# Optimization experiments

Hardware: AMD Instinct MI355X
Metric: run time of the kernel (lower is better)

The kernel has to match this reference:

```python
import jax, jax.numpy as jnp
import numpy as np

B, S, D, M = 4, 2048, 1024, 4  # batch, seq_len, d_model, n_stride_masks


def setup_inputs() -> dict:
    key = jax.random.key(0)
    ks = jax.random.split(key, 10)
    lin = lambda k: jax.random.normal(k, (D, D), jnp.float32) / np.float32(np.sqrt(D))
    return {
        "x": jax.random.normal(ks[0], (B, S, D), jnp.float32),
        "stride_masks": jax.random.randint(ks[1], (M, S, S), 0, 2, jnp.int32),
        "Wq": lin(ks[2]), "bq": jnp.zeros((D,), jnp.float32),
        "Wk": lin(ks[3]), "bk": jnp.zeros((D,), jnp.float32),
        "Wv": lin(ks[4]), "bv": jnp.zeros((D,), jnp.float32),
        "Wo": lin(ks[5]), "bo": jnp.zeros((D,), jnp.float32),
    }


def reference(x, stride_masks, Wq, bq, Wk, bk, Wv, bv, Wo, bo):
    scale = jnp.float32(np.sqrt(D))
    Q = x @ Wq + bq  # [B,S,D]
    K = x @ Wk + bk
    V = x @ Wv + bv
    # scores are identical for every mask; compute once (same math as the loop)
    scores = jnp.einsum("bqd,bkd->bqk", Q, K) / scale  # [B,S,S]
    masked = jnp.where(stride_masks[:, None] == 0, jnp.float32(-1e9), scores[None])  # [M,B,S,S]
    weights = jax.nn.softmax(masked, axis=-1)
    # sum over masks then divide by M == mean(stack(outs), 0)
    out = jnp.einsum("mbqk,bkd->bqd", weights, V) / jnp.float32(M)
    return out @ Wo + bo
```

## Files before the change

kernel.cpp:

```cpp
#include <hip/hip_runtime.h>
#include <hip/hip_bf16.h>
#include <stdint.h>

#define B_ 4
#define S_ 2048
#define D_ 1024
#define M_ 4

typedef __bf16 bf16;
typedef _Float16 f16;
typedef unsigned char u8;
typedef __bf16 bf16x8 __attribute__((ext_vector_type(8)));
typedef _Float16 f16x8 __attribute__((ext_vector_type(8)));
typedef float f32x4 __attribute__((ext_vector_type(4)));

__device__ __forceinline__ void async_copy16(const void* g, void* l) {
  __builtin_amdgcn_global_load_lds(
      (const __attribute__((address_space(1))) void*)g,
      (__attribute__((address_space(3))) void*)l, 16, 0, 0);
}

__global__ __launch_bounds__(256) void prep(
    const float* __restrict__ x, const float* __restrict__ w0,
    const float* __restrict__ w1, const float* __restrict__ w2,
    const float* __restrict__ w3, const int* __restrict__ masks,
    bf16* __restrict__ xc, bf16* __restrict__ WT, u8* __restrict__ pk) {
  __shared__ bf16 t[64][65];
  const int blk = blockIdx.x;
  const int tid = threadIdx.x;
  const long SS = (long)S_ * S_;

  if (blk < 4096) {
    const long i = (long)blk * 2048 + tid * 8;
    const float4 a = *(const float4*)(x + i);
    const float4 b = *(const float4*)(x + i + 4);
    bf16x8 o;
    o[0] = (bf16)a.x; o[1] = (bf16)a.y; o[2] = (bf16)a.z; o[3] = (bf16)a.w;
    o[4] = (bf16)b.x; o[5] = (bf16)b.y; o[6] = (bf16)b.z; o[7] = (bf16)b.w;
    *(bf16x8*)(xc + i) = o;
  } else if (blk < 5120) {
    const int local = blk - 4096;
    const int z = local >> 8;
    const int rem = local & 255;
    const int r0 = (rem >> 4) * 64;
    const int c0 = (rem & 15) * 64;
    const int tx = tid & 63;
    const int ty = tid >> 6;
    const float* in = (z == 0) ? w0 : (z == 1) ? w1 : (z == 2) ? w2 : w3;
    bf16* out = WT + (long)z * D_ * D_;
    for (int i = ty; i < 64; i += 4)
      t[i][tx] = (bf16)in[(long)(r0 + i) * D_ + c0 + tx];
    __syncthreads();
    for (int i = ty; i < 64; i += 4)
      out[(long)(c0 + i) * D_ + r0 + tx] = t[tx][i];
  } else {
    const long e = (long)(blk - 5120) * 2048 + tid * 8;
    unsigned long long wv = 0;
#pragma unroll
    for (int m = 0; m < M_; ++m) {
      const int4 a = *(const int4*)(masks + m * SS + e);
      const int4 b = *(const int4*)(masks + m * SS + e + 4);
      const int v[8] = {a.x, a.y, a.z, a.w, b.x, b.y, b.z, b.w};
#pragma unroll
      for (int j = 0; j < 8; ++j)
        wv |= (unsigned long long)(v[j] != 0 ? 1u : 0u) << (8 * j + m);
    }
    *(unsigned long long*)(pk + e) = wv;
  }
}

__global__ __launch_bounds__(256) void transposeB(
    const bf16* __restrict__ in, bf16* __restrict__ out,
    int rows, int cols, long ib, long ob) {
  __shared__ bf16 t[64][65];
  in += (long)blockIdx.z * ib;
  out += (long)blockIdx.z * ob;
  const int r0 = blockIdx.y * 64;
  const int c0 = blockIdx.x * 64;
  const int tx = threadIdx.x & 63;
  const int ty = threadIdx.x >> 6;
#pragma unroll
  for (int i = ty; i < 64; i += 4) t[i][tx] = in[(long)(r0 + i) * cols + c0 + tx];
  __syncthreads();
#pragma unroll
  for (int i = ty; i < 64; i += 4) out[(long)(c0 + i) * rows + r0 + tx] = t[tx][i];
}

#define MODE_PLAIN 0
#define MODE_EXP 1
#define MODE_QKV 2

template <typename OutT, int MODE>
__global__ __launch_bounds__(256) void gemm_bt(
    const bf16* __restrict__ A, long aB, int lda,
    const bf16* __restrict__ Bt, long bB, int ldb,
    OutT* __restrict__ C, long cB, int ldc,
    const float* __restrict__ bias0, const float* __restrict__ bias1,
    const float* __restrict__ bias2, float alpha, int K) {
  __shared__ __align__(16) bf16 As[2][128 * 64];
  __shared__ __align__(16) bf16 Bs[2][128 * 64];
  const int tid = threadIdx.x;
  const int lane = tid & 63;
  const int w = tid >> 6;
  const int wm = w & 1;
  const int wn = w >> 1;
  A += (long)blockIdx.z * aB;
  Bt += (long)blockIdx.z * bB;
  if (MODE != MODE_QKV) C += (long)blockIdx.z * cB;

  const int gx = gridDim.x;
  const int pid = blockIdx.y * gx + blockIdx.x;
  const int gsz = 16 * gx;
  const int bym = (pid / gsz) * 16 + (pid % 16);
  const int bxm = (pid % gsz) / 16;

  const int row0 = bym * 128;
  const int col0 = bxm * 128;
  const int quad = lane >> 4;
  const int l15 = lane & 15;
  const int srow = lane >> 3;
  const int scol = (lane & 7) * 8;

  f32x4 acc[4][4];
#pragma unroll
  for (int i = 0; i < 4; ++i)
#pragma unroll
    for (int j = 0; j < 4; ++j) acc[i][j] = (f32x4){0.f, 0.f, 0.f, 0.f};

  const int nk = K >> 6;

#pragma unroll
  for (int c = 0; c < 4; ++c) {
    const int r = c * 32 + w * 8;
    async_copy16(A + (long)(row0 + r + srow) * lda + scol, &As[0][r * 64]);
    async_copy16(Bt + (long)(col0 + r + srow) * ldb + scol, &Bs[0][r * 64]);
  }

  for (int i = 0; i < nk; ++i) {
    const int cur = i & 1;
    __syncthreads();
    if (i + 1 < nk) {
      const int kt = (i + 1) << 6;
      const int nxt = cur ^ 1;
#pragma unroll
      for (int c = 0; c < 4; ++c) {
        const int r = c * 32 + w * 8;
        async_copy16(A + (long)(row0 + r + srow) * lda + kt + scol, &As[nxt][r * 64]);
        async_copy16(Bt + (long)(col0 + r + srow) * ldb + kt + scol, &Bs[nxt][r * 64]);
      }
    }
#pragma unroll
    for (int ks = 0; ks < 2; ++ks) {
      bf16x8 af[4], bf[4];
#pragma unroll
      for (int j = 0; j < 4; ++j) {
        af[j] = *(const bf16x8*)&As[cur][(wm * 64 + j * 16 + l15) * 64 + ks * 32 + quad * 8];
        bf[j] = *(const bf16x8*)&Bs[cur][(wn * 64 + j * 16 + l15) * 64 + ks * 32 + quad * 8];
      }
#pragma unroll
      for (int mi = 0; mi < 4; ++mi)
#pragma unroll
        for (int ni = 0; ni < 4; ++ni)
          acc[mi][ni] = __builtin_amdgcn_mfma_f32_16x16x32_bf16(af[mi], bf[ni], acc[mi][ni], 0, 0, 0);
    }
  }

  const int grp = (MODE == MODE_QKV) ? (bxm >> 3) : 0;
  const float* bias = (MODE == MODE_QKV)
                          ? (grp == 0 ? bias0 : grp == 1 ? bias1 : bias2)
                          : bias0;
  const long NX = (long)B_ * S_ * D_;

#pragma unroll
  for (int mi = 0; mi < 4; ++mi)
#pragma unroll
    for (int ni = 0; ni < 4; ++ni) {
      const int col = col0 + wn * 64 + ni * 16 + l15;
      const int lcol = col & (D_ - 1);
      const float bv = bias ? bias[MODE == MODE_QKV ? lcol : col] : 0.0f;
#pragma unroll
      for (int r = 0; r < 4; ++r) {
        const int row = row0 + wm * 64 + mi * 16 + quad * 4 + r;
        const float val = acc[mi][ni][r] * alpha + bv;
        if (MODE == MODE_EXP) {
          C[(long)row * ldc + col] = (OutT)__expf(val);
        } else if (MODE == MODE_QKV) {
          C[grp * NX + (long)row * D_ + lcol] = (OutT)val;
        } else {
          C[(long)row * ldc + col] = (OutT)val;
        }
      }
    }
}

__global__ __launch_bounds__(256) void softmax_combine(
    const f16* __restrict__ E, const u8* __restrict__ pk, bf16* __restrict__ P) {
  const int q = blockIdx.x;
  const int b = blockIdx.y;
  const int tid = threadIdx.x;
  const int lane = tid & 63;
  const int wv = tid >> 6;
  __shared__ float4 red[4];

  float e[8];
  {
    const f16x8 h = *(const f16x8*)(E + ((long)b * S_ + q) * S_ + tid * 8);
#pragma unroll
    for (int j = 0; j < 8; ++j) e[j] = (float)h[j];
  }
  const unsigned long long mb =
      *(const unsigned long long*)(pk + (long)q * S_ + tid * 8);

  float4 s = {0.f, 0.f, 0.f, 0.f};
#pragma unroll
  for (int j = 0; j < 8; ++j) {
    const unsigned bits = (unsigned)(mb >> (8 * j)) & 0xF;
    const float ev = e[j];
    if (bits & 1) s.x += ev;
    if (bits & 2) s.y += ev;
    if (bits & 4) s.z += ev;
    if (bits & 8) s.w += ev;
  }
#pragma unroll
  for (int o = 32; o > 0; o >>= 1) {
    s.x += __shfl_xor(s.x, o, 64);
    s.y += __shfl_xor(s.y, o, 64);
    s.z += __shfl_xor(s.z, o, 64);
    s.w += __shfl_xor(s.w, o, 64);
  }
  if (lane == 0) red[wv] = s;
  __syncthreads();
  const float4 t0 = red[0], t1 = red[1], t2 = red[2], t3 = red[3];
  const float r0 = 0.25f / (t0.x + t1.x + t2.x + t3.x);
  const float r1 = 0.25f / (t0.y + t1.y + t2.y + t3.y);
  const float r2 = 0.25f / (t0.z + t1.z + t2.z + t3.z);
  const float r3 = 0.25f / (t0.w + t1.w + t2.w + t3.w);

  bf16x8 o;
#pragma unroll
  for (int j = 0; j < 8; ++j) {
    const unsigned bits = (unsigned)(mb >> (8 * j)) & 0xF;
    const float wgt = ((bits & 1) ? r0 : 0.f) + ((bits & 2) ? r1 : 0.f) +
                      ((bits & 4) ? r2 : 0.f) + ((bits & 8) ? r3 : 0.f);
    o[j] = (bf16)(e[j] * wgt);
  }
  *(bf16x8*)(P + ((long)b * S_ + q) * S_ + tid * 8) = o;
}

extern "C" void kernel_launch(void* const* d_in, const int* in_sizes, int n_in,
                              void* d_out, int out_size, void* d_ws, size_t ws_size,
                              hipStream_t stream) {
  const float* x = (const float*)d_in[0];
  const int* masks = (const int*)d_in[1];
  const float* bq = (const float*)d_in[3];
  const float* bk = (const float*)d_in[5];
  const float* bv = (const float*)d_in[7];
  const float* bo = (const float*)d_in[9];
  float* out = (float*)d_out;

  const long DD = (long)D_ * D_;
  const long SD = (long)S_ * D_;
  const long NX = (long)B_ * SD;
  const long SS = (long)S_ * S_;

  bf16* xc = (bf16*)d_ws;
  bf16* WqT = xc + NX;
  bf16* WoT = WqT + 3 * DD;
  u8* pk = (u8*)(WoT + DD);
  bf16* Q = (bf16*)(pk + SS);
  bf16* K = Q + NX;
  bf16* V = K + NX;
  bf16* VT = V + NX;
  bf16* P = VT + NX;
  f16* E = (f16*)(P + (long)B_ * SS);
  bf16* attn = Q;

  dim3 blk(256);

  prep<<<dim3(7168), blk, 0, stream>>>(
      x, (const float*)d_in[2], (const float*)d_in[4], (const float*)d_in[6],
      (const float*)d_in[8], masks, xc, WqT, pk);

  gemm_bt<bf16, MODE_QKV><<<dim3(24, 64), blk, 0, stream>>>(
      xc, 0, D_, WqT, 0, D_, Q, 0, D_, bq, bk, bv, 1.0f, D_);

  transposeB<<<dim3(16, 32, B_), blk, 0, stream>>>(V, VT, S_, D_, SD, SD);

  gemm_bt<f16, MODE_EXP><<<dim3(16, 16, B_), blk, 0, stream>>>(
      Q, SD, D_, K, SD, D_, E, SS, S_, nullptr, nullptr, nullptr, 1.0f / 32.0f, D_);

  softmax_combine<<<dim3(S_, B_), blk, 0, stream>>>(E, pk, P);

  gemm_bt<bf16, MODE_PLAIN><<<dim3(8, 16, B_), blk, 0, stream>>>(
      P, SS, S_, VT, SD, S_, attn, SD, D_, nullptr, nullptr, nullptr, 1.0f, S_);

  gemm_bt<float, MODE_PLAIN><<<dim3(8, 64), blk, 0, stream>>>(
      attn, 0, D_, WoT, 0, D_, out, 0, D_, bo, nullptr, nullptr, 1.0f, D_);
}
```

Baseline: 399.7 us.

## Add 256x256-tile 8-wave GEMM with interleaved async staging for QKV and scores

Introduces a new GEMM kernel using 256x256 output tiles, 512 threads, double-buffered LDS split into two k-halves, with global-to-LDS async copies interleaved between MFMA phases, plus s_setprio around the MFMA bursts. It replaces the QKV projection and QK^T score GEMMs, aiming for more data reuse per tile and better overlap of loads with compute. The large tiles use 128KB of LDS and many accumulator registers, so occupancy drops to one block per CU and grids shrink (384 and 256 blocks), which risks poor CU utilization on the smaller score grid.

```diff
diff --git a/kernel.cpp b/kernel.cpp
--- a/kernel.cpp
+++ b/kernel.cpp
@@ -193,6 +193,170 @@
     }
 }
 
+__device__ __forceinline__ void stage_half(const bf16* __restrict__ G, int ld,
+                                           int row_base, int kcol,
+                                           bf16* region, int tid) {
+  const int r = tid >> 2;
+  const int c = ((tid & 3) ^ ((tid >> 3) & 3)) << 3;
+  const bf16* g = G + (long)(row_base + r) * ld + kcol + c;
+  bf16* dst = region + ((tid >> 6) << 9);
+  async_copy16(g, dst);
+  async_copy16(g + (long)128 * ld, dst + 4096);
+}
+
+template <typename OutT, int MODE>
+__global__ __launch_bounds__(512) void gemm256(
+    const bf16* __restrict__ A, long aB, int lda,
+    const bf16* __restrict__ Bt, long bB, int ldb,
+    OutT* __restrict__ C, long cB, int ldc,
+    const float* __restrict__ bias0, const float* __restrict__ bias1,
+    const float* __restrict__ bias2, float alpha, int K) {
+  __shared__ __align__(16) bf16 As[2][2][256 * 32];
+  __shared__ __align__(16) bf16 Bs[2][2][256 * 32];
+  const int tid = threadIdx.x;
+  const int lane = tid & 63;
+  const int w = tid >> 6;
+  const int wm = w & 1;
+  const int wn = w >> 1;
+  const int quad = lane >> 4;
+  const int l15 = lane & 15;
+  const int fse = (quad ^ ((l15 >> 1) & 3)) << 3;
+
+  A += (long)blockIdx.z * aB;
+  Bt += (long)blockIdx.z * bB;
+  if (MODE != MODE_QKV) C += (long)blockIdx.z * cB;
+
+  const int gx = gridDim.x;
+  const int pid = blockIdx.y * gx + blockIdx.x;
+  const int gsz = 8 * gx;
+  const int bym = (pid / gsz) * 8 + (pid % 8);
+  const int bxm = (pid % gsz) / 8;
+  const int row0 = bym * 256;
+  const int col0 = bxm * 256;
+
+  f32x4 acc[8][4];
+#pragma unroll
+  for (int i = 0; i < 8; ++i)
+#pragma unroll
+    for (int j = 0; j < 4; ++j) acc[i][j] = (f32x4){0.f, 0.f, 0.f, 0.f};
+
+  const int nk = K >> 6;
+
+  stage_half(A, lda, row0, 0, &As[0][0][0], tid);
+  stage_half(Bt, ldb, col0, 0, &Bs[0][0][0], tid);
+  stage_half(A, lda, row0, 32, &As[0][1][0], tid);
+  stage_half(Bt, ldb, col0, 32, &Bs[0][1][0], tid);
+  if (nk > 1) {
+    stage_half(A, lda, row0, 64, &As[1][0][0], tid);
+    stage_half(Bt, ldb, col0, 64, &Bs[1][0][0], tid);
+    asm volatile("s_waitcnt vmcnt(4)" ::: "memory");
+  } else {
+    asm volatile("s_waitcnt vmcnt(0)" ::: "memory");
+  }
+  __builtin_amdgcn_s_barrier();
+
+  for (int t = 0; t < nk; ++t) {
+    const int buf = t & 1;
+    bf16x8 af[8], b0, b1;
+
+#pragma unroll
+    for (int m = 0; m < 8; ++m)
+      af[m] = *(const bf16x8*)&As[buf][0][(wm * 128 + m * 16 + l15) * 32 + fse];
+    b0 = *(const bf16x8*)&Bs[buf][0][(wn * 64 + l15) * 32 + fse];
+    b1 = *(const bf16x8*)&Bs[buf][0][(wn * 64 + 16 + l15) * 32 + fse];
+    if (t + 1 < nk)
+      stage_half(A, lda, row0, ((t + 1) << 6) + 32, &As[buf ^ 1][1][0], tid);
+    __builtin_amdgcn_s_barrier();
+    asm volatile("s_waitcnt lgkmcnt(0)");
+    __builtin_amdgcn_s_setprio(1);
+#pragma unroll
+    for (int m = 0; m < 8; ++m) {
+      acc[m][0] = __builtin_amdgcn_mfma_f32_16x16x32_bf16(af[m], b0, acc[m][0], 0, 0, 0);
+      acc[m][1] = __builtin_amdgcn_mfma_f32_16x16x32_bf16(af[m], b1, acc[m][1], 0, 0, 0);
+    }
+    __builtin_amdgcn_s_setprio(0);
+    __builtin_amdgcn_s_barrier();
+
+    b0 = *(const bf16x8*)&Bs[buf][0][(wn * 64 + 32 + l15) * 32 + fse];
+    b1 = *(const bf16x8*)&Bs[buf][0][(wn * 64 + 48 + l15) * 32 + fse];
+    if (t + 1 < nk)
+      stage_half(Bt, ldb, col0, ((t + 1) << 6) + 32, &Bs[buf ^ 1][1][0], tid);
+    __builtin_amdgcn_s_barrier();
+    asm volatile("s_waitcnt lgkmcnt(0)");
+    __builtin_amdgcn_s_setprio(1);
+#pragma unroll
+    for (int m = 0; m < 8; ++m) {
+      acc[m][2] = __builtin_amdgcn_mfma_f32_16x16x32_bf16(af[m], b0, acc[m][2], 0, 0, 0);
+      acc[m][3] = __builtin_amdgcn_mfma_f32_16x16x32_bf16(af[m], b1, acc[m][3], 0, 0, 0);
+    }
+    __builtin_amdgcn_s_setprio(0);
+    __builtin_amdgcn_s_barrier();
+
+#pragma unroll
+    for (int m = 0; m < 8; ++m)
+      af[m] = *(const bf16x8*)&As[buf][1][(wm * 128 + m * 16 + l15) * 32 + fse];
+    b0 = *(const bf16x8*)&Bs[buf][1][(wn * 64 + l15) * 32 + fse];
+    b1 = *(const bf16x8*)&Bs[buf][1][(wn * 64 + 16 + l15) * 32 + fse];
+    if (t + 2 < nk)
+      stage_half(A, lda, row0, (t + 2) << 6, &As[buf][0][0], tid);
+    __builtin_amdgcn_s_barrier();
+    asm volatile("s_waitcnt lgkmcnt(0)");
+    __builtin_amdgcn_s_setprio(1);
+#pragma unroll
+    for (int m = 0; m < 8; ++m) {
+      acc[m][0] = __builtin_amdgcn_mfma_f32_16x16x32_bf16(af[m], b0, acc[m][0], 0, 0, 0);
+      acc[m][1] = __builtin_amdgcn_mfma_f32_16x16x32_bf16(af[m], b1, acc[m][1], 0, 0, 0);
+    }
+    __builtin_amdgcn_s_setprio(0);
+    __builtin_amdgcn_s_barrier();
+
+    b0 = *(const bf16x8*)&Bs[buf][1][(wn * 64 + 32 + l15) * 32 + fse];
+    b1 = *(const bf16x8*)&Bs[buf][1][(wn * 64 + 48 + l15) * 32 + fse];
+    if (t + 2 < nk)
+      stage_half(Bt, ldb, col0, (t + 2) << 6, &Bs[buf][0][0], tid);
+    if (t + 2 < nk)
+      asm volatile("s_waitcnt vmcnt(4)" ::: "memory");
+    else
+      asm volatile("s_waitcnt vmcnt(0)" ::: "memory");
+    __builtin_amdgcn_s_barrier();
+    asm volatile("s_waitcnt lgkmcnt(0)");
+    __builtin_amdgcn_s_setprio(1);
+#pragma unroll
+    for (int m = 0; m < 8; ++m) {
+      acc[m][2] = __builtin_amdgcn_mfma_f32_16x16x32_bf16(af[m], b0, acc[m][2], 0, 0, 0);
+      acc[m][3] = __builtin_amdgcn_mfma_f32_16x16x32_bf16(af[m], b1, acc[m][3], 0, 0, 0);
+    }
+    __builtin_amdgcn_s_setprio(0);
+    __builtin_amdgcn_s_barrier();
+  }
+
+  const int grp = (MODE == MODE_QKV) ? (bxm >> 2) : 0;
+  const float* bias = (MODE == MODE_QKV)
+                          ? (grp == 0 ? bias0 : grp == 1 ? bias1 : bias2)
+                          : bias0;
+  const long NX = (long)B_ * S_ * D_;
+#pragma unroll
+  for (int mi = 0; mi < 8; ++mi)
+#pragma unroll
+    for (int ni = 0; ni < 4; ++ni) {
+      const int col = col0 + wn * 64 + ni * 16 + l15;
+      const int lcol = col & (D_ - 1);
+      const float bv = bias ? bias[MODE == MODE_QKV ? lcol : col] : 0.0f;
+#pragma unroll
+      for (int r = 0; r < 4; ++r) {
+        const int row = row0 + wm * 128 + mi * 16 + quad * 4 + r;
+        const float val = acc[mi][ni][r] * alpha + bv;
+        if (MODE == MODE_EXP) {
+          C[(long)row * ldc + col] = (OutT)__expf(val);
+        } else if (MODE == MODE_QKV) {
+          C[grp * NX + (long)row * D_ + lcol] = (OutT)val;
+        } else {
+          C[(long)row * ldc + col] = (OutT)val;
+        }
+      }
+    }
+}
+
 __global__ __launch_bounds__(256) void softmax_combine(
     const f16* __restrict__ E, const u8* __restrict__ pk, bf16* __restrict__ P) {
   const int q = blockIdx.x;
@@ -276,17 +440,18 @@
   bf16* attn = Q;
 
   dim3 blk(256);
+  dim3 blk512(512);
 
   prep<<<dim3(7168), blk, 0, stream>>>(
       x, (const float*)d_in[2], (const float*)d_in[4], (const float*)d_in[6],
       (const float*)d_in[8], masks, xc, WqT, pk);
 
-  gemm_bt<bf16, MODE_QKV><<<dim3(24, 64), blk, 0, stream>>>(
+  gemm256<bf16, MODE_QKV><<<dim3(12, 32), blk512, 0, stream>>>(
       xc, 0, D_, WqT, 0, D_, Q, 0, D_, bq, bk, bv, 1.0f, D_);
 
   transposeB<<<dim3(16, 32, B_), blk, 0, stream>>>(V, VT, S_, D_, SD, SD);
 
-  gemm_bt<f16, MODE_EXP><<<dim3(16, 16, B_), blk, 0, stream>>>(
+  gemm256<f16, MODE_EXP><<<dim3(8, 8, B_), blk512, 0, stream>>>(
       Q, SD, D_, K, SD, D_, E, SS, S_, nullptr, nullptr, nullptr, 1.0f / 32.0f, D_);
 
   softmax_combine<<<dim3(S_, B_), blk, 0, stream>>>(E, pk, P);
```

New measurement: 371.5 us. 1.08x faster.

## Rewrite GEMM as 256x128 tiles with 512 threads and deeper async pipeline

Applied to the files above, without the earlier changes.

Replaces the 128x128 double-buffered GEMM with a 256x128 tile kernel using 8 waves. It splits K into 32-wide half-stages with a three-deep async global-to-LDS prefetch driven by manual vmcnt waits and raw barriers. LDS reads use an XOR swizzle to avoid bank conflicts, and MFMA blocks are wrapped in setprio. Batched launches are folded into the row dimension, so each GEMM call becomes a 2D grid. The aim is to hide memory latency and raise MFMA utilization, at the cost of more LDS and registers and fragile hand-written waitcnt logic.

```diff
diff --git a/kernel.cpp b/kernel.cpp
--- a/kernel.cpp
+++ b/kernel.cpp
@@ -89,37 +89,80 @@
 #define MODE_PLAIN 0
 #define MODE_EXP 1
 #define MODE_QKV 2
+#define MODE_PV 3
 
 template <typename OutT, int MODE>
-__global__ __launch_bounds__(256) void gemm_bt(
-    const bf16* __restrict__ A, long aB, int lda,
-    const bf16* __restrict__ Bt, long bB, int ldb,
-    OutT* __restrict__ C, long cB, int ldc,
+__global__ __launch_bounds__(512) void gemmA(
+    const bf16* __restrict__ A, int lda,
+    const bf16* __restrict__ Bt, long bzs, int ldb,
+    OutT* __restrict__ C, int ldc,
     const float* __restrict__ bias0, const float* __restrict__ bias1,
     const float* __restrict__ bias2, float alpha, int K) {
-  __shared__ __align__(16) bf16 As[2][128 * 64];
-  __shared__ __align__(16) bf16 Bs[2][128 * 64];
+  __shared__ __align__(16) bf16 As[2][2][256 * 32];
+  __shared__ __align__(16) bf16 Bs[2][2][128 * 32];
   const int tid = threadIdx.x;
   const int lane = tid & 63;
   const int w = tid >> 6;
-  const int wm = w & 1;
-  const int wn = w >> 1;
-  A += (long)blockIdx.z * aB;
-  Bt += (long)blockIdx.z * bB;
-  if (MODE != MODE_QKV) C += (long)blockIdx.z * cB;
+  const int wm = w & 3;
+  const int wn = w >> 2;
+  const int quad = lane >> 4;
+  const int l15 = lane & 15;
+  const int fse = (quad ^ ((l15 >> 1) & 3)) << 3;
 
   const int gx = gridDim.x;
   const int pid = blockIdx.y * gx + blockIdx.x;
-  const int gsz = 16 * gx;
-  const int bym = (pid / gsz) * 16 + (pid % 16);
-  const int bxm = (pid % gsz) / 16;
-
-  const int row0 = bym * 128;
+  const int gsz = 8 * gx;
+  const int bym = (pid / gsz) * 8 + (pid % 8);
+  const int bxm = (pid % gsz) / 8;
+  const int row0 = bym * 256;
   const int col0 = bxm * 128;
-  const int quad = lane >> 4;
-  const int l15 = lane & 15;
-  const int srow = lane >> 3;
-  const int scol = (lane & 7) * 8;
+
+  const bf16* Arow = A + (long)row0 * lda;
+  const bf16* Bcol;
+  int grp = 0;
+  if (MODE == MODE_QKV) {
+    grp = col0 >> 10;
+    Bcol = Bt + (long)grp * ((long)D_ * D_) + (long)(col0 & (D_ - 1)) * ldb;
+  } else if (MODE == MODE_PV || MODE == MODE_EXP) {
+    Bcol = Bt + (long)(row0 >> 11) * bzs + (long)col0 * ldb;
+  } else {
+    Bcol = Bt + (long)col0 * ldb;
+  }
+
+  const int sr = tid >> 2;
+  const int sc = ((tid & 3) ^ ((tid >> 3) & 3)) << 3;
+  const bf16* gA = Arow + (long)sr * lda + sc;
+  const bf16* gB = Bcol + (long)sr * ldb + sc;
+  const int dstoff = (tid >> 6) << 9;
+  const long a128 = (long)128 * lda;
+
+#define STAGE(h)                                                       \
+  {                                                                    \
+    const int kc_ = (h) * 32;                                          \
+    bf16* da_ = &As[((h) >> 1) & 1][(h) & 1][0] + dstoff;              \
+    bf16* db_ = &Bs[((h) >> 1) & 1][(h) & 1][0] + dstoff;              \
+    async_copy16(gA + kc_, da_);                                       \
+    async_copy16(gA + kc_ + a128, da_ + 4096);                         \
+    async_copy16(gB + kc_, db_);                                       \
+  }
+
+#define READF(Ra, Rb, bufv, ksv)                                           \
+  {                                                                        \
+    const bf16* pa_ = &As[bufv][ksv][0];                                   \
+    const bf16* pb_ = &Bs[bufv][ksv][0];                                   \
+    _Pragma("unroll") for (int j = 0; j < 4; ++j) {                        \
+      Ra[j] = *(const bf16x8*)&pa_[(wm * 64 + j * 16 + l15) * 32 + fse];   \
+      Rb[j] = *(const bf16x8*)&pb_[(wn * 64 + j * 16 + l15) * 32 + fse];   \
+    }                                                                      \
+  }
+
+#define MM(Ra, Rb)                                                         \
+  __builtin_amdgcn_s_setprio(1);                                           \
+  _Pragma("unroll") for (int mi = 0; mi < 4; ++mi)                         \
+      _Pragma("unroll") for (int ni = 0; ni < 4; ++ni) acc[mi][ni] =       \
+          __builtin_amdgcn_mfma_f32_16x16x32_bf16(Ra[mi], Rb[ni],          \
+                                                  acc[mi][ni], 0, 0, 0);   \
+  __builtin_amdgcn_s_setprio(0);
 
   f32x4 acc[4][4];
 #pragma unroll
@@ -129,65 +172,65 @@
 
   const int nk = K >> 6;
 
-#pragma unroll
-  for (int c = 0; c < 4; ++c) {
-    const int r = c * 32 + w * 8;
-    async_copy16(A + (long)(row0 + r + srow) * lda + scol, &As[0][r * 64]);
-    async_copy16(Bt + (long)(col0 + r + srow) * ldb + scol, &Bs[0][r * 64]);
-  }
-
-  for (int i = 0; i < nk; ++i) {
-    const int cur = i & 1;
-    __syncthreads();
-    if (i + 1 < nk) {
-      const int kt = (i + 1) << 6;
-      const int nxt = cur ^ 1;
-#pragma unroll
-      for (int c = 0; c < 4; ++c) {
-        const int r = c * 32 + w * 8;
-        async_copy16(A + (long)(row0 + r + srow) * lda + kt + scol, &As[nxt][r * 64]);
-        async_copy16(Bt + (long)(col0 + r + srow) * ldb + kt + scol, &Bs[nxt][r * 64]);
-      }
+  STAGE(0);
+  STAGE(1);
+  STAGE(2);
+  asm volatile("s_waitcnt vmcnt(6)" ::: "memory");
+  __builtin_amdgcn_s_barrier();
+  __builtin_amdgcn_sched_barrier(0);
+
+  bf16x8 a0[4], b0[4], a1[4], b1[4];
+  READF(a0, b0, 0, 0);
+
+  for (int t = 0; t < nk; ++t) {
+    const int buf = t & 1;
+
+    if (t + 1 < nk)
+      asm volatile("s_waitcnt vmcnt(3)" ::: "memory");
+    else
+      asm volatile("s_waitcnt vmcnt(0)" ::: "memory");
+    __builtin_amdgcn_s_barrier();
+    __builtin_amdgcn_sched_barrier(0);
+    READF(a1, b1, buf, 1);
+    if (t + 1 < nk) STAGE(2 * t + 3);
+    MM(a0, b0);
+
+    if (t + 1 < nk) {
+      asm volatile("s_waitcnt vmcnt(3)" ::: "memory");
+      __builtin_amdgcn_s_barrier();
+      __builtin_amdgcn_sched_barrier(0);
+      READF(a0, b0, buf ^ 1, 0);
+      if (t + 3 <= nk) STAGE(2 * t + 4);
     }
-#pragma unroll
-    for (int ks = 0; ks < 2; ++ks) {
-      bf16x8 af[4], bf[4];
-#pragma unroll
-      for (int j = 0; j < 4; ++j) {
-        af[j] = *(const bf16x8*)&As[cur][(wm * 64 + j * 16 + l15) * 64 + ks * 32 + quad * 8];
-        bf[j] = *(const bf16x8*)&Bs[cur][(wn * 64 + j * 16 + l15) * 64 + ks * 32 + quad * 8];
-      }
-#pragma unroll
-      for (int mi = 0; mi < 4; ++mi)
-#pragma unroll
-        for (int ni = 0; ni < 4; ++ni)
-          acc[mi][ni] = __builtin_amdgcn_mfma_f32_16x16x32_bf16(af[mi], bf[ni], acc[mi][ni], 0, 0, 0);
-    }
-  }
-
-  const int grp = (MODE == MODE_QKV) ? (bxm >> 3) : 0;
+    MM(a1, b1);
+  }
+
+#undef STAGE
+#undef READF
+#undef MM
+
   const float* bias = (MODE == MODE_QKV)
                           ? (grp == 0 ? bias0 : grp == 1 ? bias1 : bias2)
                           : bias0;
   const long NX = (long)B_ * S_ * D_;
-
+  OutT* Cb = (MODE == MODE_QKV) ? C + (long)grp * NX : C;
 #pragma unroll
   for (int mi = 0; mi < 4; ++mi)
 #pragma unroll
     for (int ni = 0; ni < 4; ++ni) {
       const int col = col0 + wn * 64 + ni * 16 + l15;
-      const int lcol = col & (D_ - 1);
-      const float bv = bias ? bias[MODE == MODE_QKV ? lcol : col] : 0.0f;
+      const int ccol = (MODE == MODE_QKV) ? (col & (D_ - 1)) : col;
+      const float bv = bias ? bias[ccol] : 0.0f;
 #pragma unroll
       for (int r = 0; r < 4; ++r) {
         const int row = row0 + wm * 64 + mi * 16 + quad * 4 + r;
         const float val = acc[mi][ni][r] * alpha + bv;
         if (MODE == MODE_EXP) {
-          C[(long)row * ldc + col] = (OutT)__expf(val);
+          Cb[(long)row * ldc + col] = (OutT)__expf(val);
         } else if (MODE == MODE_QKV) {
-          C[grp * NX + (long)row * D_ + lcol] = (OutT)val;
+          Cb[(long)row * D_ + ccol] = (OutT)val;
         } else {
-          C[(long)row * ldc + col] = (OutT)val;
+          Cb[(long)row * ldc + col] = (OutT)val;
         }
       }
     }
@@ -276,24 +319,25 @@
   bf16* attn = Q;
 
   dim3 blk(256);
+  dim3 blk512(512);
 
   prep<<<dim3(7168), blk, 0, stream>>>(
       x, (const float*)d_in[2], (const float*)d_in[4], (const float*)d_in[6],
       (const float*)d_in[8], masks, xc, WqT, pk);
 
-  gemm_bt<bf16, MODE_QKV><<<dim3(24, 64), blk, 0, stream>>>(
-      xc, 0, D_, WqT, 0, D_, Q, 0, D_, bq, bk, bv, 1.0f, D_);
+  gemmA<bf16, MODE_QKV><<<dim3(24, 32), blk512, 0, stream>>>(
+      xc, D_, WqT, 0, D_, Q, D_, bq, bk, bv, 1.0f, D_);
 
   transposeB<<<dim3(16, 32, B_), blk, 0, stream>>>(V, VT, S_, D_, SD, SD);
 
-  gemm_bt<f16, MODE_EXP><<<dim3(16, 16, B_), blk, 0, stream>>>(
-      Q, SD, D_, K, SD, D_, E, SS, S_, nullptr, nullptr, nullptr, 1.0f / 32.0f, D_);
+  gemmA<f16, MODE_EXP><<<dim3(16, 32), blk512, 0, stream>>>(
+      Q, D_, K, SD, D_, E, S_, nullptr, nullptr, nullptr, 1.0f / 32.0f, D_);
 
   softmax_combine<<<dim3(S_, B_), blk, 0, stream>>>(E, pk, P);
 
-  gemm_bt<bf16, MODE_PLAIN><<<dim3(8, 16, B_), blk, 0, stream>>>(
-      P, SS, S_, VT, SD, S_, attn, SD, D_, nullptr, nullptr, nullptr, 1.0f, S_);
-
-  gemm_bt<float, MODE_PLAIN><<<dim3(8, 64), blk, 0, stream>>>(
-      attn, 0, D_, WoT, 0, D_, out, 0, D_, bo, nullptr, nullptr, 1.0f, D_);
-}
+  gemmA<bf16, MODE_PV><<<dim3(8, 32), blk512, 0, stream>>>(
+      P, S_, VT, SD, S_, attn, D_, nullptr, nullptr, nullptr, 1.0f, S_);
+
+  gemmA<float, MODE_PLAIN><<<dim3(8, 32), blk512, 0, stream>>>(
+      attn, D_, WoT, 0, D_, out, D_, bo, nullptr, nullptr, 1.0f, D_);
+}
```

Result: faster. 365.8 us (-8.5%).
